# Performance work log

Hardware: AMD Instinct MI355X
Metric: run time of the kernel (lower is better)

Reference implementation:

```python
import jax, jax.numpy as jnp
import numpy as np

R, S, RO, H, KD, VD = 14, 2, 7, 8, 32, 64  # resolution, stride, res_out, heads, key_dim, val_dim
EPS = 1e-5
SCALE = KD ** -0.5


def _bias_idxs():
    i = np.arange(R)
    kp = np.stack(np.meshgrid(i, i, indexing='ij')).reshape(2, -1)          # (2, 196)
    qi = np.arange(0, R, S)
    qp = np.stack(np.meshgrid(qi, qi, indexing='ij')).reshape(2, -1)        # (2, 49)
    rel = np.abs(qp[:, :, None] - kp[:, None, :])                           # (2, 49, 196)
    return jnp.asarray(rel[0] * R + rel[1], dtype=jnp.int32)                # (49, 196)

BIAS_IDXS = _bias_idxs()


def linear_norm(x, w, g, b, m, v):
    # Linear (no bias) followed by BatchNorm1d in eval mode (running stats)
    inv = g * jax.lax.rsqrt(v + EPS)
    return (x @ w.T) * inv + (b - m * inv)


def hardswish(x):
    return x * jnp.clip(x + 3.0, 0.0, 6.0) * (1.0 / 6.0)


def setup_inputs() -> dict:
    key = jax.random.key(0)
    ks = jax.random.split(key, 12)
    d = {
        'x': jax.random.normal(ks[0], (256, 196, 256), jnp.float32),
        'kv_w': jax.random.normal(ks[1], (768, 256), jnp.float32) * 0.02,
        'kv_g': jax.random.uniform(ks[2], (768,), jnp.float32, 0.5, 1.5),
        'kv_b': jax.random.normal(ks[3], (768,), jnp.float32) * 0.02,
        'kv_m': jax.random.normal(ks[4], (768,), jnp.float32) * 0.01,
        'kv_v': jax.random.uniform(ks[5], (768,), jnp.float32, 0.5, 1.5),
        'q_w': jax.random.normal(ks[6], (256, 256), jnp.float32) * 0.02,
        'q_g': jax.random.uniform(ks[7], (256,), jnp.float32, 0.5, 1.5),
        'q_b': jax.random.normal(ks[8], (256,), jnp.float32) * 0.02,
        'q_m': jax.random.normal(ks[9], (256,), jnp.float32) * 0.01,
        'q_v': jax.random.uniform(ks[10], (256,), jnp.float32, 0.5, 1.5),
        'proj_w': jax.random.normal(ks[11], (384, 512), jnp.float32) * 0.02,
        'proj_g': jnp.ones((384,), jnp.float32),
        'proj_b': jnp.zeros((384,), jnp.float32),
        'proj_m': jnp.zeros((384,), jnp.float32),
        'proj_v': jnp.ones((384,), jnp.float32),
        'attn_bias': jax.random.normal(jax.random.fold_in(key, 99), (H, R * R), jnp.float32) * 0.02,
    }
    return d


def reference(x, kv_w, kv_g, kv_b, kv_m, kv_v,
              q_w, q_g, q_b, q_m, q_v,
              proj_w, proj_g, proj_b, proj_m, proj_v, attn_bias):
    B, N, C = x.shape  # (B, 196, 256)
    kv = linear_norm(x, kv_w, kv_g, kv_b, kv_m, kv_v)          # (B, N, 768)
    kv = kv.reshape(B, N, H, KD + VD)                          # per-head split
    k = kv[..., :KD].transpose(0, 2, 3, 1)                     # (B, H, KD, N)
    v = kv[..., KD:].transpose(0, 2, 1, 3)                     # (B, H, N, VD)
    # Subsample queries on the 14x14 grid with stride 2 -> 49 tokens
    xq = x.reshape(B, R, R, C)[:, ::S, ::S].reshape(B, RO * RO, C)
    q = linear_norm(xq, q_w, q_g, q_b, q_m, q_v)               # (B, 49, 256)
    q = q.reshape(B, RO * RO, H, KD).transpose(0, 2, 1, 3)     # (B, H, 49, KD)
    bias = attn_bias[:, BIAS_IDXS]                             # (H, 49, 196)
    scores = jnp.einsum('bhqd,bhdn->bhqn', q, k) * SCALE + bias
    attn = jax.nn.softmax(scores, axis=-1)                     # (B, H, 49, 196)
    out = jnp.einsum('bhqn,bhnv->bhqv', attn, v)               # (B, H, 49, VD)
    out = out.transpose(0, 2, 1, 3).reshape(B, RO * RO, H * VD)  # (B, 49, 512)
    return linear_norm(hardswish(out), proj_w, proj_g, proj_b, proj_m, proj_v)  # (B, 49, 384)
```

## Files before the change

### kernel.cpp

```cpp
#include <hip/hip_runtime.h>

#define EPS 1e-5f
#define QK_SCALE 0.17677669529663687f

typedef __attribute__((ext_vector_type(8))) short bf16x8;
typedef __attribute__((ext_vector_type(4))) float f32x4;

__device__ inline unsigned short bf16_rne(float f) {
    unsigned int u = __float_as_uint(f);
    u = u + 0x7FFFu + ((u >> 16) & 1u);
    return (unsigned short)(u >> 16);
}
__device__ inline float bf16_f(unsigned short s) {
    return __uint_as_float(((unsigned int)s) << 16);
}
__device__ inline void split1(float v, unsigned short& hi, unsigned short& lo) {
    hi = bf16_rne(v); lo = bf16_rne(v - bf16_f(hi));
}

__device__ inline unsigned int cvtpk_bf16(float a, float b) {
    unsigned int r;
    asm("v_cvt_pk_bf16_f32 %0, %1, %2" : "=v"(r) : "v"(a), "v"(b));
    return r;
}
__device__ inline void split2pk(float a, float b, unsigned int& h, unsigned int& l) {
    h = cvtpk_bf16(a, b);
    float ra = a - __uint_as_float(h << 16);
    float rb = b - __uint_as_float(h & 0xFFFF0000u);
    l = cvtpk_bf16(ra, rb);
}
__device__ inline void split4pk(float4 v, uint2& h, uint2& l) {
    unsigned int h01, l01, h23, l23;
    split2pk(v.x, v.y, h01, l01);
    split2pk(v.z, v.w, h23, l23);
    h.x = h01; h.y = h23; l.x = l01; l.y = l23;
}

#define MFMA16(a, b, c) __builtin_amdgcn_mfma_f32_16x16x32_bf16((a), (b), (c), 0, 0, 0)

__global__ __launch_bounds__(256)
void prep_split(const float* __restrict__ kv_w, const float* __restrict__ q_w,
                const float* __restrict__ pw,
                unsigned short* __restrict__ wb_hi, unsigned short* __restrict__ wb_lo,
                unsigned short* __restrict__ pw_hi, unsigned short* __restrict__ pw_lo)
{
    int i = blockIdx.x * 256 + threadIdx.x;
    if (i < 262144) {
        int c = i & 255, j = (i >> 8) & 127, h = i >> 15;
        float v = (j < 96) ? kv_w[(h * 96 + j) * 256 + c]
                           : q_w[(h * 32 + (j - 96)) * 256 + c];
        unsigned short hi, lo; split1(v, hi, lo);
        wb_hi[i] = hi; wb_lo[i] = lo;
    } else {
        int p = i - 262144;
        if (p < 196608) {
            float v = pw[p];
            unsigned short hi, lo; split1(v, hi, lo);
            pw_hi[p] = hi; pw_lo[p] = lo;
        }
    }
}

__global__ __launch_bounds__(1024, 4)
void levit_fused_attn(const float* __restrict__ x,
                      const unsigned short* __restrict__ wb_hi,
                      const unsigned short* __restrict__ wb_lo,
                      const float* __restrict__ kv_g, const float* __restrict__ kv_b,
                      const float* __restrict__ kv_m, const float* __restrict__ kv_v,
                      const float* __restrict__ q_g, const float* __restrict__ q_b,
                      const float* __restrict__ q_m, const float* __restrict__ q_v,
                      const float* __restrict__ attn_bias,
                      unsigned short* __restrict__ ao_hi,
                      unsigned short* __restrict__ ao_lo)
{
    __shared__ __align__(16) unsigned short s_big[80192];
    __shared__ float bias_s[196];
    __shared__ float nrm_iv[128];
    __shared__ float nrm_be[128];

    unsigned short* s_phi = s_big;
    unsigned short* s_plo = s_big + 14848;
    unsigned short* s_khi = s_big + 29696;
    unsigned short* s_klo = s_big + 38016;
    unsigned short* s_qhi = s_big + 46336;
    unsigned short* s_qlo = s_big + 48416;
    unsigned short* s_vhi = s_big + 50496;
    unsigned short* s_vlo = s_big + 65344;
    unsigned short* st_xhi = s_big;
    unsigned short* st_xlo = s_big + 14976;
    unsigned short* st_whi = s_big + 29952;
    unsigned short* st_wlo = s_big + 39168;

    const int t = threadIdx.x;
    const int b = blockIdx.x;
    const int hh = blockIdx.y;

    const int l = t & 63;
    const int w = t >> 6;
    const int rg = w & 3;
    const int cg = w >> 2;
    const int lrow = l & 15;
    const int kg = (l >> 4) * 8;
    const int g4 = (l >> 4) * 4;

    const int wj = t >> 3, wc8 = (t & 7) * 8;
    const unsigned short* wsrc_hi = wb_hi + (hh * 128 + wj) * 256 + wc8;
    const unsigned short* wsrc_lo = wb_lo + (hh * 128 + wj) * 256 + wc8;
    const float* xbase = x + b * 196 * 256;
    const float4 f4z = {0.f, 0.f, 0.f, 0.f};

    float4 xr[4]; bf16x8 wrh, wrl;

    #pragma unroll
    for (int it = 0; it < 4; ++it) {
        const int f = t + 1024 * it;
        const int row = f >> 4, c4 = (f & 15) * 4;
        xr[it] = f4z;
        if (row < 196) xr[it] = *(const float4*)&xbase[row * 256 + c4];
    }
    wrh = *(const bf16x8*)&wsrc_hi[0];
    wrl = *(const bf16x8*)&wsrc_lo[0];

    if (t < 196) bias_s[t] = attn_bias[hh * 196 + t];
    if (t >= 256 && t < 384) {
        int jj = t - 256;
        float gg, bb, mm, vv;
        if (jj < 96) { int col = hh * 96 + jj;        gg = kv_g[col]; bb = kv_b[col]; mm = kv_m[col]; vv = kv_v[col]; }
        else         { int col = hh * 32 + (jj - 96); gg = q_g[col];  bb = q_b[col];  mm = q_m[col];  vv = q_v[col]; }
        float iv = gg * rsqrtf(vv + EPS);
        nrm_iv[jj] = iv; nrm_be[jj] = bb - mm * iv;
    }
    for (int i = t; i < 64 * 36; i += 1024) {
        int r = i / 36, c = 196 + i % 36;
        s_vhi[r * 232 + c] = 0; s_vlo[r * 232 + c] = 0;
    }

    f32x4 acc[4][2];
    #pragma unroll
    for (int i = 0; i < 4; ++i) { acc[i][0] = (f32x4){0,0,0,0}; acc[i][1] = (f32x4){0,0,0,0}; }

    #pragma unroll
    for (int it = 0; it < 4; ++it) {
        const int f = t + 1024 * it;
        const int row = f >> 4, c4 = (f & 15) * 4;
        if (row < 208) {
            uint2 h2, l2; split4pk(xr[it], h2, l2);
            *(uint2*)&st_xhi[row * 72 + c4] = h2;
            *(uint2*)&st_xlo[row * 72 + c4] = l2;
        }
    }
    *(bf16x8*)&st_whi[wj * 72 + wc8] = wrh;
    *(bf16x8*)&st_wlo[wj * 72 + wc8] = wrl;
    __syncthreads();

    for (int s = 0; s < 4; ++s) {
        if (s < 3) {
            const int kcn = 64 * (s + 1);
            #pragma unroll
            for (int it = 0; it < 4; ++it) {
                const int f = t + 1024 * it;
                const int row = f >> 4, c4 = (f & 15) * 4;
                xr[it] = f4z;
                if (row < 196) xr[it] = *(const float4*)&xbase[row * 256 + kcn + c4];
            }
            wrh = *(const bf16x8*)&wsrc_hi[kcn];
            wrl = *(const bf16x8*)&wsrc_lo[kcn];
        }

        #pragma unroll
        for (int sub = 0; sub < 2; ++sub) {
            const int ko = 32 * sub + kg;
            bf16x8 wfh[2], wfl[2];
            #pragma unroll
            for (int ctl = 0; ctl < 2; ++ctl) {
                const int jr = 16 * (2 * cg + ctl) + lrow;
                wfh[ctl] = *(const bf16x8*)&st_whi[jr * 72 + ko];
                wfl[ctl] = *(const bf16x8*)&st_wlo[jr * 72 + ko];
            }
            #pragma unroll
            for (int i = 0; i < 4; ++i) {
                const int rt = rg + 4 * i;
                if (rt < 13) {
                    const int arow = 16 * rt + lrow;
                    bf16x8 xh = *(const bf16x8*)&st_xhi[arow * 72 + ko];
                    bf16x8 xl = *(const bf16x8*)&st_xlo[arow * 72 + ko];
                    #pragma unroll
                    for (int ctl = 0; ctl < 2; ++ctl) {
                        acc[i][ctl] = MFMA16(wfh[ctl], xh, acc[i][ctl]);
                        acc[i][ctl] = MFMA16(wfh[ctl], xl, acc[i][ctl]);
                        acc[i][ctl] = MFMA16(wfl[ctl], xh, acc[i][ctl]);
                    }
                }
            }
        }

        if (s < 3) {
            __syncthreads();
            #pragma unroll
            for (int it = 0; it < 4; ++it) {
                const int f = t + 1024 * it;
                const int row = f >> 4, c4 = (f & 15) * 4;
                if (row < 208) {
                    uint2 h2, l2; split4pk(xr[it], h2, l2);
                    *(uint2*)&st_xhi[row * 72 + c4] = h2;
                    *(uint2*)&st_xlo[row * 72 + c4] = l2;
                }
            }
            *(bf16x8*)&st_whi[wj * 72 + wc8] = wrh;
            *(bf16x8*)&st_wlo[wj * 72 + wc8] = wrl;
            __syncthreads();
        }
    }
    __syncthreads();

    #pragma unroll
    for (int ctl = 0; ctl < 2; ++ctl) {
        const int ct = 2 * cg + ctl;
        const int j0 = 16 * ct + g4;
        const float iv0 = nrm_iv[j0+0], be0 = nrm_be[j0+0];
        const float iv1 = nrm_iv[j0+1], be1 = nrm_be[j0+1];
        const float iv2 = nrm_iv[j0+2], be2 = nrm_be[j0+2];
        const float iv3 = nrm_iv[j0+3], be3 = nrm_be[j0+3];
        #pragma unroll
        for (int i = 0; i < 4; ++i) {
            const int rt = rg + 4 * i;
            if (rt < 13) {
                const int n = 16 * rt + lrow;
                if (n < 196) {
                    float v0 = acc[i][ctl][0] * iv0 + be0;
                    float v1 = acc[i][ctl][1] * iv1 + be1;
                    float v2 = acc[i][ctl][2] * iv2 + be2;
                    float v3 = acc[i][ctl][3] * iv3 + be3;
                    unsigned int h01, l01, h23, l23;
                    split2pk(v0, v1, h01, l01);
                    split2pk(v2, v3, h23, l23);
                    if (ct < 2) {
                        *(uint2*)&s_khi[n * 40 + j0] = (uint2){h01, h23};
                        *(uint2*)&s_klo[n * 40 + j0] = (uint2){l01, l23};
                    } else if (ct < 6) {
                        const int vd0 = j0 - 32;
                        s_vhi[(vd0+0) * 232 + n] = (unsigned short)h01;
                        s_vhi[(vd0+1) * 232 + n] = (unsigned short)(h01 >> 16);
                        s_vhi[(vd0+2) * 232 + n] = (unsigned short)h23;
                        s_vhi[(vd0+3) * 232 + n] = (unsigned short)(h23 >> 16);
                        s_vlo[(vd0+0) * 232 + n] = (unsigned short)l01;
                        s_vlo[(vd0+1) * 232 + n] = (unsigned short)(l01 >> 16);
                        s_vlo[(vd0+2) * 232 + n] = (unsigned short)l23;
                        s_vlo[(vd0+3) * 232 + n] = (unsigned short)(l23 >> 16);
                    } else {
                        const int a = n / 28, rem = n - 28 * a;
                        if (rem < 14 && !(rem & 1)) {
                            const int qi = a * 7 + (rem >> 1);
                            *(uint2*)&s_qhi[qi * 40 + (j0 - 96)] = (uint2){h01, h23};
                            *(uint2*)&s_qlo[qi * 40 + (j0 - 96)] = (uint2){l01, l23};
                        }
                    }
                }
            }
        }
    }
    __syncthreads();

    for (int i = t; i < 64 * 24; i += 1024) {
        int r = i / 24, c = 208 + i % 24;
        s_phi[r * 232 + c] = 0; s_plo[r * 232 + c] = 0;
    }

    if (w < 4) {
        const int mt = w;
        bf16x8 qh = *(const bf16x8*)&s_qhi[(16 * mt + lrow) * 40 + kg];
        bf16x8 ql = *(const bf16x8*)&s_qlo[(16 * mt + lrow) * 40 + kg];
        f32x4 sv[13];
        #pragma unroll
        for (int nt = 0; nt < 13; ++nt) {
            bf16x8 kh = *(const bf16x8*)&s_khi[(16 * nt + lrow) * 40 + kg];
            bf16x8 kl = *(const bf16x8*)&s_klo[(16 * nt + lrow) * 40 + kg];
            f32x4 a = {0.f, 0.f, 0.f, 0.f};
            a = MFMA16(kh, qh, a);
            a = MFMA16(kh, ql, a);
            a = MFMA16(kl, qh, a);
            sv[nt] = a;
        }
        const int m = 16 * mt + lrow;
        const int mq = m < 49 ? m : 48;
        const int yq = (mq / 7) * 2, xq2 = (mq % 7) * 2;

        float lmax = -3.0e38f;
        #pragma unroll
        for (int nt = 0; nt < 13; ++nt) {
            #pragma unroll
            for (int reg = 0; reg < 4; ++reg) {
                const int n = 16 * nt + g4 + reg;
                float sc;
                if (n < 196) {
                    const int yk = n / 14, xk = n - 14 * yk;
                    int d0 = yq - yk;  d0 = d0 < 0 ? -d0 : d0;
                    int d1 = xq2 - xk; d1 = d1 < 0 ? -d1 : d1;
                    sc = sv[nt][reg] * QK_SCALE + bias_s[d0 * 14 + d1];
                } else {
                    sc = -1.0e30f;
                }
                sv[nt][reg] = sc;
                lmax = fmaxf(lmax, sc);
            }
        }
        lmax = fmaxf(lmax, __shfl_xor(lmax, 16, 64));
        lmax = fmaxf(lmax, __shfl_xor(lmax, 32, 64));
        float rsum = 0.f;
        #pragma unroll
        for (int nt = 0; nt < 13; ++nt)
            #pragma unroll
            for (int reg = 0; reg < 4; ++reg) {
                float p = __expf(sv[nt][reg] - lmax);
                sv[nt][reg] = p;
                rsum += p;
            }
        rsum += __shfl_xor(rsum, 16, 64);
        rsum += __shfl_xor(rsum, 32, 64);
        const float rinv = 1.f / rsum;
        #pragma unroll
        for (int nt = 0; nt < 13; ++nt) {
            unsigned int h01, l01, h23, l23;
            split2pk(sv[nt][0] * rinv, sv[nt][1] * rinv, h01, l01);
            split2pk(sv[nt][2] * rinv, sv[nt][3] * rinv, h23, l23);
            const int o = m * 232 + 16 * nt + g4;
            *(uint2*)&s_phi[o] = (uint2){h01, h23};
            *(uint2*)&s_plo[o] = (uint2){l01, l23};
        }
    }
    __syncthreads();

    {
        const int mtv = w & 3;
        const int ntv = w >> 2;
        f32x4 pacc = {0.f, 0.f, 0.f, 0.f};
        #pragma unroll
        for (int s = 0; s < 7; ++s) {
            bf16x8 ph = *(const bf16x8*)&s_phi[(16 * mtv + lrow) * 232 + 32 * s + kg];
            bf16x8 pl = *(const bf16x8*)&s_plo[(16 * mtv + lrow) * 232 + 32 * s + kg];
            bf16x8 vh = *(const bf16x8*)&s_vhi[(16 * ntv + lrow) * 232 + 32 * s + kg];
            bf16x8 vl = *(const bf16x8*)&s_vlo[(16 * ntv + lrow) * 232 + 32 * s + kg];
            pacc = MFMA16(vh, ph, pacc);
            pacc = MFMA16(vh, pl, pacc);
            pacc = MFMA16(vl, ph, pacc);
        }
        const int m = 16 * mtv + lrow;
        if (m < 49) {
            const int vd0 = 16 * ntv + g4;
            float hs0, hs1, hs2, hs3;
            { float v = pacc[0]; hs0 = v * fminf(fmaxf(v + 3.f, 0.f), 6.f) * (1.f/6.f); }
            { float v = pacc[1]; hs1 = v * fminf(fmaxf(v + 3.f, 0.f), 6.f) * (1.f/6.f); }
            { float v = pacc[2]; hs2 = v * fminf(fmaxf(v + 3.f, 0.f), 6.f) * (1.f/6.f); }
            { float v = pacc[3]; hs3 = v * fminf(fmaxf(v + 3.f, 0.f), 6.f) * (1.f/6.f); }
            unsigned int h01, l01, h23, l23;
            split2pk(hs0, hs1, h01, l01);
            split2pk(hs2, hs3, h23, l23);
            const int idx = ((b * 49 + m) * 8 + hh) * 64 + vd0;
            *(uint2*)&ao_hi[idx] = (uint2){h01, h23};
            *(uint2*)&ao_lo[idx] = (uint2){l01, l23};
        }
    }
}

__global__ __launch_bounds__(512, 2)
void levit_proj(const unsigned short* __restrict__ ao_hi,
                const unsigned short* __restrict__ ao_lo,
                const unsigned short* __restrict__ pw_hi,
                const unsigned short* __restrict__ pw_lo,
                const float* __restrict__ pg, const float* __restrict__ pb,
                const float* __restrict__ pm, const float* __restrict__ pv,
                float* __restrict__ out)
{
    __shared__ __align__(16) unsigned short s_a[2 * 64 * 72];
    __shared__ __align__(16) unsigned short s_w[2 * 96 * 72];

    unsigned short* s_ahi = s_a;          unsigned short* s_alo = s_a + 64 * 72;
    unsigned short* s_whi = s_w;          unsigned short* s_wlo = s_w + 96 * 72;

    const int t = threadIdx.x;
    const int b = blockIdx.x;
    const int cg = blockIdx.y;
    const int l = t & 63;
    const int w = t >> 6;
    const int lrow = l & 15;
    const int kg = (l >> 4) * 8;
    const int g4 = (l >> 4) * 4;

    f32x4 acc[3] = {{0.f,0.f,0.f,0.f},{0.f,0.f,0.f,0.f},{0.f,0.f,0.f,0.f}};

    for (int kc = 0; kc < 512; kc += 64) {
        __syncthreads();
        #pragma unroll
        for (int it = 0; it < 2; ++it) {
            int f = t + 512 * it;
            int plane = f >> 9, rem = f & 511;
            int r = rem >> 3, c8 = (rem & 7) * 8;
            const unsigned short* src = plane ? ao_lo : ao_hi;
            unsigned short* dst = plane ? s_alo : s_ahi;
            bf16x8 v = {};
            if (r < 49) v = *(const bf16x8*)&src[(b * 49 + r) * 512 + kc + c8];
            *(bf16x8*)&dst[r * 72 + c8] = v;
        }
        #pragma unroll
        for (int it = 0; it < 3; ++it) {
            int f = t + 512 * it;
            int plane = (f >= 768), rem = plane ? f - 768 : f;
            int r = rem >> 3, c8 = (rem & 7) * 8;
            const unsigned short* src = plane ? pw_lo : pw_hi;
            unsigned short* dst = plane ? s_wlo : s_whi;
            *(bf16x8*)&dst[r * 72 + c8] =
                *(const bf16x8*)&src[(cg * 96 + r) * 512 + kc + c8];
        }
        __syncthreads();
        #pragma unroll
        for (int sub = 0; sub < 2; ++sub) {
            int ko = 32 * sub + kg;
            #pragma unroll
            for (int i = 0; i < 3; ++i) {
                int tid3 = 3 * w + i;
                int mt = tid3 & 3, nt = tid3 >> 2;
                bf16x8 ah = *(const bf16x8*)&s_ahi[(16 * mt + lrow) * 72 + ko];
                bf16x8 al = *(const bf16x8*)&s_alo[(16 * mt + lrow) * 72 + ko];
                bf16x8 bh = *(const bf16x8*)&s_whi[(16 * nt + lrow) * 72 + ko];
                bf16x8 bl = *(const bf16x8*)&s_wlo[(16 * nt + lrow) * 72 + ko];
                acc[i] = MFMA16(ah, bh, acc[i]);
                acc[i] = MFMA16(ah, bl, acc[i]);
                acc[i] = MFMA16(al, bh, acc[i]);
            }
        }
    }

    #pragma unroll
    for (int i = 0; i < 3; ++i) {
        int tid3 = 3 * w + i;
        int mt = tid3 & 3, nt = tid3 >> 2;
        int o = cg * 96 + 16 * nt + lrow;
        float iv = pg[o] * rsqrtf(pv[o] + EPS);
        float be = pb[o] - pm[o] * iv;
        #pragma unroll
        for (int reg = 0; reg < 4; ++reg) {
            int r = 16 * mt + g4 + reg;
            if (r < 49) out[(b * 49 + r) * 384 + o] = acc[i][reg] * iv + be;
        }
    }
}

extern "C" void kernel_launch(void* const* d_in, const int* in_sizes, int n_in,
                              void* d_out, int out_size, void* d_ws, size_t ws_size,
                              hipStream_t stream) {
    const float* x     = (const float*)d_in[0];
    const float* kv_w  = (const float*)d_in[1];
    const float* kv_g  = (const float*)d_in[2];
    const float* kv_b  = (const float*)d_in[3];
    const float* kv_m  = (const float*)d_in[4];
    const float* kv_v  = (const float*)d_in[5];
    const float* q_wp  = (const float*)d_in[6];
    const float* q_g   = (const float*)d_in[7];
    const float* q_b   = (const float*)d_in[8];
    const float* q_m   = (const float*)d_in[9];
    const float* q_v   = (const float*)d_in[10];
    const float* pw    = (const float*)d_in[11];
    const float* pg    = (const float*)d_in[12];
    const float* pb    = (const float*)d_in[13];
    const float* pm    = (const float*)d_in[14];
    const float* pv    = (const float*)d_in[15];
    const float* ab    = (const float*)d_in[16];

    unsigned short* ao_hi = (unsigned short*)d_ws;
    unsigned short* ao_lo = ao_hi + 12544 * 512;
    unsigned short* wb_hi = ao_lo + 12544 * 512;
    unsigned short* wb_lo = wb_hi + 262144;
    unsigned short* pw_hi = wb_lo + 262144;
    unsigned short* pw_lo = pw_hi + 196608;

    prep_split<<<1792, 256, 0, stream>>>(kv_w, q_wp, pw, wb_hi, wb_lo, pw_hi, pw_lo);

    dim3 g1(256, 8);
    levit_fused_attn<<<g1, 1024, 0, stream>>>(x, wb_hi, wb_lo,
                                              kv_g, kv_b, kv_m, kv_v,
                                              q_g, q_b, q_m, q_v, ab, ao_hi, ao_lo);
    levit_proj<<<dim3(256, 4), 512, 0, stream>>>(ao_hi, ao_lo, pw_hi, pw_lo,
                                                 pg, pb, pm, pv, (float*)d_out);
}
```

Measured before the change: 297.4 us.

## Transpose V-wave MFMA operands for vectorized V stores; widen x staging loads

Waves that compute V columns now swap the MFMA A/B operands, so each lane holds four consecutive tokens for one value dim. V can then go to shared memory with 64-bit vector stores instead of eight scalar 16-bit transposed stores. The x staging now loads eight floats per thread with 128-bit LDS writes and fewer iterations. The zero-fill of the P padding moves onto waves that sit idle during softmax. The cost is wave-divergent code paths and more complex indexing.

```diff
diff --git a/kernel.cpp b/kernel.cpp
--- a/kernel.cpp
+++ b/kernel.cpp
@@ -99,24 +99,29 @@
     const int w = t >> 6;
     const int rg = w & 3;
     const int cg = w >> 2;
+    const bool vwave = (cg == 1 || cg == 2);
     const int lrow = l & 15;
     const int kg = (l >> 4) * 8;
     const int g4 = (l >> 4) * 4;
 
+    const int x0row = t >> 3,          x0c8 = (t & 7) * 8;
+    const int u1 = t + 1024;
+    const int x1row = u1 >> 3,         x1c8 = (u1 & 7) * 8;
+    const bool xv1 = (t < 640);
     const int wj = t >> 3, wc8 = (t & 7) * 8;
     const unsigned short* wsrc_hi = wb_hi + (hh * 128 + wj) * 256 + wc8;
     const unsigned short* wsrc_lo = wb_lo + (hh * 128 + wj) * 256 + wc8;
     const float* xbase = x + b * 196 * 256;
     const float4 f4z = {0.f, 0.f, 0.f, 0.f};
 
-    float4 xr[4]; bf16x8 wrh, wrl;
-
-    #pragma unroll
-    for (int it = 0; it < 4; ++it) {
-        const int f = t + 1024 * it;
-        const int row = f >> 4, c4 = (f & 15) * 4;
-        xr[it] = f4z;
-        if (row < 196) xr[it] = *(const float4*)&xbase[row * 256 + c4];
+    float4 x0a, x0b, x1a, x1b; bf16x8 wrh, wrl;
+
+    x0a = (x0row < 196) ? *(const float4*)&xbase[x0row * 256 + x0c8]     : f4z;
+    x0b = (x0row < 196) ? *(const float4*)&xbase[x0row * 256 + x0c8 + 4] : f4z;
+    x1a = f4z; x1b = f4z;
+    if (xv1 && x1row < 196) {
+        x1a = *(const float4*)&xbase[x1row * 256 + x1c8];
+        x1b = *(const float4*)&xbase[x1row * 256 + x1c8 + 4];
     }
     wrh = *(const bf16x8*)&wsrc_hi[0];
     wrl = *(const bf16x8*)&wsrc_lo[0];
@@ -139,14 +144,15 @@
     #pragma unroll
     for (int i = 0; i < 4; ++i) { acc[i][0] = (f32x4){0,0,0,0}; acc[i][1] = (f32x4){0,0,0,0}; }
 
-    #pragma unroll
-    for (int it = 0; it < 4; ++it) {
-        const int f = t + 1024 * it;
-        const int row = f >> 4, c4 = (f & 15) * 4;
-        if (row < 208) {
-            uint2 h2, l2; split4pk(xr[it], h2, l2);
-            *(uint2*)&st_xhi[row * 72 + c4] = h2;
-            *(uint2*)&st_xlo[row * 72 + c4] = l2;
+    {
+        uint2 ha, la, hb, lb;
+        split4pk(x0a, ha, la); split4pk(x0b, hb, lb);
+        *(uint4*)&st_xhi[x0row * 72 + x0c8] = (uint4){ha.x, ha.y, hb.x, hb.y};
+        *(uint4*)&st_xlo[x0row * 72 + x0c8] = (uint4){la.x, la.y, lb.x, lb.y};
+        if (xv1) {
+            split4pk(x1a, ha, la); split4pk(x1b, hb, lb);
+            *(uint4*)&st_xhi[x1row * 72 + x1c8] = (uint4){ha.x, ha.y, hb.x, hb.y};
+            *(uint4*)&st_xlo[x1row * 72 + x1c8] = (uint4){la.x, la.y, lb.x, lb.y};
         }
     }
     *(bf16x8*)&st_whi[wj * 72 + wc8] = wrh;
@@ -156,12 +162,12 @@
     for (int s = 0; s < 4; ++s) {
         if (s < 3) {
             const int kcn = 64 * (s + 1);
-            #pragma unroll
-            for (int it = 0; it < 4; ++it) {
-                const int f = t + 1024 * it;
-                const int row = f >> 4, c4 = (f & 15) * 4;
-                xr[it] = f4z;
-                if (row < 196) xr[it] = *(const float4*)&xbase[row * 256 + kcn + c4];
+            x0a = (x0row < 196) ? *(const float4*)&xbase[x0row * 256 + kcn + x0c8]     : f4z;
+            x0b = (x0row < 196) ? *(const float4*)&xbase[x0row * 256 + kcn + x0c8 + 4] : f4z;
+            x1a = f4z; x1b = f4z;
+            if (xv1 && x1row < 196) {
+                x1a = *(const float4*)&xbase[x1row * 256 + kcn + x1c8];
+                x1b = *(const float4*)&xbase[x1row * 256 + kcn + x1c8 + 4];
             }
             wrh = *(const bf16x8*)&wsrc_hi[kcn];
             wrl = *(const bf16x8*)&wsrc_lo[kcn];
@@ -184,11 +190,20 @@
                     const int arow = 16 * rt + lrow;
                     bf16x8 xh = *(const bf16x8*)&st_xhi[arow * 72 + ko];
                     bf16x8 xl = *(const bf16x8*)&st_xlo[arow * 72 + ko];
-                    #pragma unroll
-                    for (int ctl = 0; ctl < 2; ++ctl) {
-                        acc[i][ctl] = MFMA16(wfh[ctl], xh, acc[i][ctl]);
-                        acc[i][ctl] = MFMA16(wfh[ctl], xl, acc[i][ctl]);
-                        acc[i][ctl] = MFMA16(wfl[ctl], xh, acc[i][ctl]);
+                    if (vwave) {
+                        #pragma unroll
+                        for (int ctl = 0; ctl < 2; ++ctl) {
+                            acc[i][ctl] = MFMA16(xh, wfh[ctl], acc[i][ctl]);
+                            acc[i][ctl] = MFMA16(xl, wfh[ctl], acc[i][ctl]);
+                            acc[i][ctl] = MFMA16(xh, wfl[ctl], acc[i][ctl]);
+                        }
+                    } else {
+                        #pragma unroll
+                        for (int ctl = 0; ctl < 2; ++ctl) {
+                            acc[i][ctl] = MFMA16(wfh[ctl], xh, acc[i][ctl]);
+                            acc[i][ctl] = MFMA16(wfh[ctl], xl, acc[i][ctl]);
+                            acc[i][ctl] = MFMA16(wfl[ctl], xh, acc[i][ctl]);
+                        }
                     }
                 }
             }
@@ -196,15 +211,14 @@
 
         if (s < 3) {
             __syncthreads();
-            #pragma unroll
-            for (int it = 0; it < 4; ++it) {
-                const int f = t + 1024 * it;
-                const int row = f >> 4, c4 = (f & 15) * 4;
-                if (row < 208) {
-                    uint2 h2, l2; split4pk(xr[it], h2, l2);
-                    *(uint2*)&st_xhi[row * 72 + c4] = h2;
-                    *(uint2*)&st_xlo[row * 72 + c4] = l2;
-                }
+            uint2 ha, la, hb, lb;
+            split4pk(x0a, ha, la); split4pk(x0b, hb, lb);
+            *(uint4*)&st_xhi[x0row * 72 + x0c8] = (uint4){ha.x, ha.y, hb.x, hb.y};
+            *(uint4*)&st_xlo[x0row * 72 + x0c8] = (uint4){la.x, la.y, lb.x, lb.y};
+            if (xv1) {
+                split4pk(x1a, ha, la); split4pk(x1b, hb, lb);
+                *(uint4*)&st_xhi[x1row * 72 + x1c8] = (uint4){ha.x, ha.y, hb.x, hb.y};
+                *(uint4*)&st_xlo[x1row * 72 + x1c8] = (uint4){la.x, la.y, lb.x, lb.y};
             }
             *(bf16x8*)&st_whi[wj * 72 + wc8] = wrh;
             *(bf16x8*)&st_wlo[wj * 72 + wc8] = wrl;
@@ -213,46 +227,54 @@
     }
     __syncthreads();
 
-    #pragma unroll
-    for (int ctl = 0; ctl < 2; ++ctl) {
-        const int ct = 2 * cg + ctl;
-        const int j0 = 16 * ct + g4;
-        const float iv0 = nrm_iv[j0+0], be0 = nrm_be[j0+0];
-        const float iv1 = nrm_iv[j0+1], be1 = nrm_be[j0+1];
-        const float iv2 = nrm_iv[j0+2], be2 = nrm_be[j0+2];
-        const float iv3 = nrm_iv[j0+3], be3 = nrm_be[j0+3];
-        #pragma unroll
-        for (int i = 0; i < 4; ++i) {
-            const int rt = rg + 4 * i;
-            if (rt < 13) {
-                const int n = 16 * rt + lrow;
-                if (n < 196) {
-                    float v0 = acc[i][ctl][0] * iv0 + be0;
-                    float v1 = acc[i][ctl][1] * iv1 + be1;
-                    float v2 = acc[i][ctl][2] * iv2 + be2;
-                    float v3 = acc[i][ctl][3] * iv3 + be3;
-                    unsigned int h01, l01, h23, l23;
-                    split2pk(v0, v1, h01, l01);
-                    split2pk(v2, v3, h23, l23);
-                    if (ct < 2) {
-                        *(uint2*)&s_khi[n * 40 + j0] = (uint2){h01, h23};
-                        *(uint2*)&s_klo[n * 40 + j0] = (uint2){l01, l23};
-                    } else if (ct < 6) {
-                        const int vd0 = j0 - 32;
-                        s_vhi[(vd0+0) * 232 + n] = (unsigned short)h01;
-                        s_vhi[(vd0+1) * 232 + n] = (unsigned short)(h01 >> 16);
-                        s_vhi[(vd0+2) * 232 + n] = (unsigned short)h23;
-                        s_vhi[(vd0+3) * 232 + n] = (unsigned short)(h23 >> 16);
-                        s_vlo[(vd0+0) * 232 + n] = (unsigned short)l01;
-                        s_vlo[(vd0+1) * 232 + n] = (unsigned short)(l01 >> 16);
-                        s_vlo[(vd0+2) * 232 + n] = (unsigned short)l23;
-                        s_vlo[(vd0+3) * 232 + n] = (unsigned short)(l23 >> 16);
-                    } else {
-                        const int a = n / 28, rem = n - 28 * a;
-                        if (rem < 14 && !(rem & 1)) {
-                            const int qi = a * 7 + (rem >> 1);
-                            *(uint2*)&s_qhi[qi * 40 + (j0 - 96)] = (uint2){h01, h23};
-                            *(uint2*)&s_qlo[qi * 40 + (j0 - 96)] = (uint2){l01, l23};
+    if (vwave) {
+        #pragma unroll
+        for (int ctl = 0; ctl < 2; ++ctl) {
+            const int ct = 2 * cg + ctl;
+            const int j = 16 * ct + lrow;
+            const int vd = j - 32;
+            const float iv = nrm_iv[j], be = nrm_be[j];
+            #pragma unroll
+            for (int i = 0; i < 4; ++i) {
+                const int rt = rg + 4 * i;
+                if (rt < 13) {
+                    const int n0 = 16 * rt + g4;
+                    if (n0 < 196) {
+                        unsigned int h01, l01, h23, l23;
+                        split2pk(acc[i][ctl][0] * iv + be, acc[i][ctl][1] * iv + be, h01, l01);
+                        split2pk(acc[i][ctl][2] * iv + be, acc[i][ctl][3] * iv + be, h23, l23);
+                        *(uint2*)&s_vhi[vd * 232 + n0] = (uint2){h01, h23};
+                        *(uint2*)&s_vlo[vd * 232 + n0] = (uint2){l01, l23};
+                    }
+                }
+            }
+        }
+    } else {
+        #pragma unroll
+        for (int ctl = 0; ctl < 2; ++ctl) {
+            const int ct = 2 * cg + ctl;
+            const int j0 = 16 * ct + g4;
+            const float4 iv4 = *(const float4*)&nrm_iv[j0];
+            const float4 be4 = *(const float4*)&nrm_be[j0];
+            #pragma unroll
+            for (int i = 0; i < 4; ++i) {
+                const int rt = rg + 4 * i;
+                if (rt < 13) {
+                    const int n = 16 * rt + lrow;
+                    if (n < 196) {
+                        unsigned int h01, l01, h23, l23;
+                        split2pk(acc[i][ctl][0] * iv4.x + be4.x, acc[i][ctl][1] * iv4.y + be4.y, h01, l01);
+                        split2pk(acc[i][ctl][2] * iv4.z + be4.z, acc[i][ctl][3] * iv4.w + be4.w, h23, l23);
+                        if (ct < 2) {
+                            *(uint2*)&s_khi[n * 40 + j0] = (uint2){h01, h23};
+                            *(uint2*)&s_klo[n * 40 + j0] = (uint2){l01, l23};
+                        } else {
+                            const int a = n / 28, rem = n - 28 * a;
+                            if (rem < 14 && !(rem & 1)) {
+                                const int qi = a * 7 + (rem >> 1);
+                                *(uint2*)&s_qhi[qi * 40 + (j0 - 96)] = (uint2){h01, h23};
+                                *(uint2*)&s_qlo[qi * 40 + (j0 - 96)] = (uint2){l01, l23};
+                            }
                         }
                     }
                 }
@@ -260,11 +282,6 @@
         }
     }
     __syncthreads();
-
-    for (int i = t; i < 64 * 24; i += 1024) {
-        int r = i / 24, c = 208 + i % 24;
-        s_phi[r * 232 + c] = 0; s_plo[r * 232 + c] = 0;
-    }
 
     if (w < 4) {
         const int mt = w;
@@ -326,6 +343,11 @@
             const int o = m * 232 + 16 * nt + g4;
             *(uint2*)&s_phi[o] = (uint2){h01, h23};
             *(uint2*)&s_plo[o] = (uint2){l01, l23};
+        }
+    } else {
+        for (int i = t - 256; i < 64 * 24; i += 768) {
+            int r = i / 24, c = 208 + i % 24;
+            s_phi[r * 232 + c] = 0; s_plo[r * 232 + c] = 0;
         }
     }
     __syncthreads();
```

Result: slower. 303.7 us (+2.1%).

## Register-prefetch next K-chunk in proj GEMM and vectorize the epilogue stores

Applied to the files above, without the earlier changes.

The projection GEMM now loads the next 64-wide K chunk from global memory into registers while MFMAs run on the current LDS tile, then writes it to LDS between barriers. The operand order of the MFMA is swapped so each lane holds four consecutive output columns, which allows float4 BN-parameter loads and float4 output stores. Each wave now reuses its A fragment across its three N tiles, and launch bounds ask for higher occupancy. The trade-off is more register pressure from prefetch buffers against the higher occupancy target, which may cause spills.

```diff
diff --git a/kernel.cpp b/kernel.cpp
--- a/kernel.cpp
+++ b/kernel.cpp
@@ -362,7 +362,7 @@
     }
 }
 
-__global__ __launch_bounds__(512, 2)
+__global__ __launch_bounds__(512, 6)
 void levit_proj(const unsigned short* __restrict__ ao_hi,
                 const unsigned short* __restrict__ ao_lo,
                 const unsigned short* __restrict__ pw_hi,
@@ -386,61 +386,106 @@
     const int kg = (l >> 4) * 8;
     const int g4 = (l >> 4) * 4;
 
+    const int ar = t >> 3, ac8 = (t & 7) * 8;
+    const bool aval = (ar < 49);
+    const long aoff = (long)(b * 49 + ar) * 512 + ac8;
+    int wpl_[3], wr_[3], wc_[3];
+    #pragma unroll
+    for (int it = 0; it < 3; ++it) {
+        int f = t + 512 * it;
+        int plane = (f >= 768), rem = plane ? f - 768 : f;
+        wpl_[it] = plane; wr_[it] = rem >> 3; wc_[it] = (rem & 7) * 8;
+    }
+
+    bf16x8 pa_h = {}, pa_l = {}, pwr[3];
+
+    if (aval) {
+        pa_h = *(const bf16x8*)&ao_hi[aoff];
+        pa_l = *(const bf16x8*)&ao_lo[aoff];
+    }
+    #pragma unroll
+    for (int it = 0; it < 3; ++it) {
+        const unsigned short* src = wpl_[it] ? pw_lo : pw_hi;
+        pwr[it] = *(const bf16x8*)&src[(cg * 96 + wr_[it]) * 512 + wc_[it]];
+    }
+    *(bf16x8*)&s_ahi[ar * 72 + ac8] = pa_h;
+    *(bf16x8*)&s_alo[ar * 72 + ac8] = pa_l;
+    #pragma unroll
+    for (int it = 0; it < 3; ++it) {
+        unsigned short* dst = wpl_[it] ? s_wlo : s_whi;
+        *(bf16x8*)&dst[wr_[it] * 72 + wc_[it]] = pwr[it];
+    }
+    __syncthreads();
+
+    const int mt = w & 3;
+    const int ntb = 3 * (w >> 2);
+
     f32x4 acc[3] = {{0.f,0.f,0.f,0.f},{0.f,0.f,0.f,0.f},{0.f,0.f,0.f,0.f}};
 
-    for (int kc = 0; kc < 512; kc += 64) {
-        __syncthreads();
-        #pragma unroll
-        for (int it = 0; it < 2; ++it) {
-            int f = t + 512 * it;
-            int plane = f >> 9, rem = f & 511;
-            int r = rem >> 3, c8 = (rem & 7) * 8;
-            const unsigned short* src = plane ? ao_lo : ao_hi;
-            unsigned short* dst = plane ? s_alo : s_ahi;
-            bf16x8 v = {};
-            if (r < 49) v = *(const bf16x8*)&src[(b * 49 + r) * 512 + kc + c8];
-            *(bf16x8*)&dst[r * 72 + c8] = v;
-        }
-        #pragma unroll
-        for (int it = 0; it < 3; ++it) {
-            int f = t + 512 * it;
-            int plane = (f >= 768), rem = plane ? f - 768 : f;
-            int r = rem >> 3, c8 = (rem & 7) * 8;
-            const unsigned short* src = plane ? pw_lo : pw_hi;
-            unsigned short* dst = plane ? s_wlo : s_whi;
-            *(bf16x8*)&dst[r * 72 + c8] =
-                *(const bf16x8*)&src[(cg * 96 + r) * 512 + kc + c8];
-        }
-        __syncthreads();
+    for (int s = 0; s < 8; ++s) {
+        if (s < 7) {
+            const int kc = 64 * (s + 1);
+            pa_h = (bf16x8){}; pa_l = (bf16x8){};
+            if (aval) {
+                pa_h = *(const bf16x8*)&ao_hi[aoff + kc];
+                pa_l = *(const bf16x8*)&ao_lo[aoff + kc];
+            }
+            #pragma unroll
+            for (int it = 0; it < 3; ++it) {
+                const unsigned short* src = wpl_[it] ? pw_lo : pw_hi;
+                pwr[it] = *(const bf16x8*)&src[(cg * 96 + wr_[it]) * 512 + kc + wc_[it]];
+            }
+        }
+
         #pragma unroll
         for (int sub = 0; sub < 2; ++sub) {
-            int ko = 32 * sub + kg;
+            const int ko = 32 * sub + kg;
+            bf16x8 ah = *(const bf16x8*)&s_ahi[(16 * mt + lrow) * 72 + ko];
+            bf16x8 al = *(const bf16x8*)&s_alo[(16 * mt + lrow) * 72 + ko];
             #pragma unroll
             for (int i = 0; i < 3; ++i) {
-                int tid3 = 3 * w + i;
-                int mt = tid3 & 3, nt = tid3 >> 2;
-                bf16x8 ah = *(const bf16x8*)&s_ahi[(16 * mt + lrow) * 72 + ko];
-                bf16x8 al = *(const bf16x8*)&s_alo[(16 * mt + lrow) * 72 + ko];
+                const int nt = ntb + i;
                 bf16x8 bh = *(const bf16x8*)&s_whi[(16 * nt + lrow) * 72 + ko];
                 bf16x8 bl = *(const bf16x8*)&s_wlo[(16 * nt + lrow) * 72 + ko];
-                acc[i] = MFMA16(ah, bh, acc[i]);
-                acc[i] = MFMA16(ah, bl, acc[i]);
-                acc[i] = MFMA16(al, bh, acc[i]);
-            }
-        }
-    }
-
-    #pragma unroll
-    for (int i = 0; i < 3; ++i) {
-        int tid3 = 3 * w + i;
-        int mt = tid3 & 3, nt = tid3 >> 2;
-        int o = cg * 96 + 16 * nt + lrow;
-        float iv = pg[o] * rsqrtf(pv[o] + EPS);
-        float be = pb[o] - pm[o] * iv;
-        #pragma unroll
-        for (int reg = 0; reg < 4; ++reg) {
-            int r = 16 * mt + g4 + reg;
-            if (r < 49) out[(b * 49 + r) * 384 + o] = acc[i][reg] * iv + be;
+                acc[i] = MFMA16(bh, ah, acc[i]);
+                acc[i] = MFMA16(bl, ah, acc[i]);
+                acc[i] = MFMA16(bh, al, acc[i]);
+            }
+        }
+
+        if (s < 7) {
+            __syncthreads();
+            *(bf16x8*)&s_ahi[ar * 72 + ac8] = pa_h;
+            *(bf16x8*)&s_alo[ar * 72 + ac8] = pa_l;
+            #pragma unroll
+            for (int it = 0; it < 3; ++it) {
+                unsigned short* dst = wpl_[it] ? s_wlo : s_whi;
+                *(bf16x8*)&dst[wr_[it] * 72 + wc_[it]] = pwr[it];
+            }
+            __syncthreads();
+        }
+    }
+
+    const int r = 16 * mt + lrow;
+    if (r < 49) {
+        #pragma unroll
+        for (int i = 0; i < 3; ++i) {
+            const int nt = ntb + i;
+            const int o0 = cg * 96 + 16 * nt + g4;
+            const float4 g4v = *(const float4*)&pg[o0];
+            const float4 v4v = *(const float4*)&pv[o0];
+            const float4 b4v = *(const float4*)&pb[o0];
+            const float4 m4v = *(const float4*)&pm[o0];
+            float iv0 = g4v.x * rsqrtf(v4v.x + EPS);
+            float iv1 = g4v.y * rsqrtf(v4v.y + EPS);
+            float iv2 = g4v.z * rsqrtf(v4v.z + EPS);
+            float iv3 = g4v.w * rsqrtf(v4v.w + EPS);
+            float4 ov;
+            ov.x = acc[i][0] * iv0 + (b4v.x - m4v.x * iv0);
+            ov.y = acc[i][1] * iv1 + (b4v.y - m4v.y * iv1);
+            ov.z = acc[i][2] * iv2 + (b4v.z - m4v.z * iv2);
+            ov.w = acc[i][3] * iv3 + (b4v.w - m4v.w * iv3);
+            *(float4*)&out[(b * 49 + r) * 384 + o0] = ov;
         }
     }
 }
```

New measurement: 284.8 us. 4.2% less time.
